# Performance work log

Hardware: AMD Instinct MI355X
Metric: run time of the kernel (lower is better)

The kernel has to match this reference:

```python
import jax, jax.numpy as jnp
import numpy as np

B, L, H, N, NL = 32, 512, 768, 64, 4
GAIN = 1.0


def layer_norm(x, w, b, eps=1e-5):
    mu = jnp.mean(x, axis=-1, keepdims=True)
    var = jnp.mean((x - mu) ** 2, axis=-1, keepdims=True)
    return (x - mu) * jax.lax.rsqrt(var + eps) * w + b


def setup_inputs() -> dict:
    key = jax.random.key(0)
    ks = jax.random.split(key, 10)
    x = jax.random.normal(ks[0], (B, L, H), dtype=jnp.float32)
    mask = jnp.ones((B, L), dtype=jnp.int32)
    # S4D parameters per layer (stacked over NL)
    log_dt = jnp.log(10.0 ** jax.random.uniform(ks[1], (NL, H), minval=-3.0, maxval=-1.0))
    A_re = jnp.zeros((NL, H, N), dtype=jnp.float32)  # real part = -exp(0) = -1
    A_im = jnp.broadcast_to(np.pi * jnp.arange(N, dtype=jnp.float32), (NL, H, N)).copy()
    C_re = jax.random.normal(ks[2], (NL, 2, H, N), dtype=jnp.float32) * 0.5 ** 0.5
    C_im = jax.random.normal(ks[3], (NL, 2, H, N), dtype=jnp.float32) * 0.5 ** 0.5
    D = jax.random.normal(ks[4], (NL, H), dtype=jnp.float32)
    Wout = jax.random.normal(ks[5], (NL, H, H), dtype=jnp.float32) / np.sqrt(H)
    bout = jnp.zeros((NL, H), dtype=jnp.float32)
    ln1_w = jnp.ones((NL, H), dtype=jnp.float32)
    ln1_b = jnp.zeros((NL, H), dtype=jnp.float32)
    ln2_w = jnp.ones((NL, H), dtype=jnp.float32)
    ln2_b = jnp.zeros((NL, H), dtype=jnp.float32)
    return dict(x=x, mask=mask, ln1_w=ln1_w, ln1_b=ln1_b, log_dt=log_dt,
                A_re=A_re, A_im=A_im, C_re=C_re, C_im=C_im, D=D,
                Wout=Wout, bout=bout, ln2_w=ln2_w, ln2_b=ln2_b)


def bis4(u, mask_f, log_dt, A_re, A_im, C_re, C_im, D, Wout, bout):
    # u: [B, L, H] (post ln_1); mask_f: [B, L] float
    u = (u * mask_f[:, :, None]).transpose(0, 2, 1)  # [B, H, L]
    dt = jnp.exp(log_dt)  # [H]
    A = (-jnp.exp(A_re) + 1j * A_im).astype(jnp.complex64)  # [H, N]
    dtA = dt[:, None] * A  # [H, N]
    C = (C_re + 1j * C_im).astype(jnp.complex64)  # [2, H, N]
    # ZOH-style: K[d,h,l] = 2 Re sum_n C (e^{dtA}-1)/A * e^{dtA l}
    Cw = C * ((jnp.exp(dtA) - 1.0) / A)  # [2, H, N]
    V = jnp.exp(dtA[:, :, None] * jnp.arange(L, dtype=jnp.float32))  # [H, N, L]
    K = 2.0 * jnp.real(jnp.einsum('dhn,hnl->dhl', Cw, V))  # [2, H, L]
    # bidirectional kernel over circular length 2L
    k_full = (jnp.pad(K[0], ((0, 0), (0, L))) +
              jnp.pad(K[1, :, ::-1], ((0, 0), (L, 0))))  # [H, 2L]
    kf = jnp.fft.rfft(k_full, n=2 * L)           # [H, L+1]
    uf = jnp.fft.rfft(u, n=2 * L)                # [B, H, L+1]
    y = jnp.fft.irfft(uf * kf, n=2 * L)[..., :L]  # [B, H, L]
    y = y + D[:, None] * u
    y = jax.nn.gelu(y)
    y = y.transpose(0, 2, 1)  # [B, L, H]
    return jnp.einsum('blh,oh->blo', y, Wout) + bout


def reference(x, mask, ln1_w, ln1_b, log_dt, A_re, A_im, C_re, C_im, D, Wout, bout, ln2_w, ln2_b):
    mask_f = mask.astype(x.dtype)
    for i in range(NL):
        y = layer_norm(x, ln1_w[i], ln1_b[i])
        y = bis4(y, mask_f, log_dt[i], A_re[i], A_im[i], C_re[i], C_im[i], D[i], Wout[i], bout[i])
        y = layer_norm(y, ln2_w[i], ln2_b[i])
        x = x + y * GAIN
    return x
```

## Files before the change

### kernel.cpp

```cpp
#include <hip/hip_runtime.h>
#include <math.h>

#define BB 32
#define LL 512
#define HH 768
#define NN 64
#define NLAYERS 4

typedef unsigned short ushort;
typedef __attribute__((ext_vector_type(8))) short bf16x8;
typedef __attribute__((ext_vector_type(4))) float f32x4;
typedef __attribute__((ext_vector_type(4))) ushort u16x4;

static __device__ __forceinline__ ushort f2bf(float f) {
  union { float f; unsigned u; } v; v.f = f;
  unsigned r = (v.u + 0x7FFF + ((v.u >> 16) & 1)) >> 16;
  return (ushort)r;
}
static __device__ __forceinline__ float bf2f(ushort u) {
  union { unsigned u; float f; } v; v.u = ((unsigned)u) << 16; return v.f;
}
static __device__ __forceinline__ void gload16(const void* g, void* l) {
  __builtin_amdgcn_global_load_lds(
      (const __attribute__((address_space(1))) unsigned int*)g,
      (__attribute__((address_space(3))) unsigned int*)l, 16, 0, 0);
}
static __device__ __forceinline__ float hw_sin(float f) {
  float r; asm("v_sin_f32 %0, %1" : "=v"(r) : "v"(f)); return r;
}
static __device__ __forceinline__ float hw_cos(float f) {
  float r; asm("v_cos_f32 %0, %1" : "=v"(r) : "v"(f)); return r;
}

__global__ __launch_bounds__(256) void compute_k_kernel(
    const float* __restrict__ log_dt, const float* __restrict__ A_re,
    const float* __restrict__ A_im, const float* __restrict__ C_re,
    const float* __restrict__ C_im, ushort* __restrict__ rev) {
  __shared__ float4 cons[2][64][5];
  __shared__ float red[2][64][17];
  int wid = threadIdx.x >> 6, lane = threadIdx.x & 63;
  int p = wid >> 1, nh = wid & 1;
  int blk = blockIdx.x * 2 + p;
  int il = blk / HH, h = blk - il * HH;
  if (lane < 32) {
    int n = nh * 32 + lane;
    float dt = expf(log_dt[blk]);
    float a_re = -expf(A_re[(size_t)blk * NN + n]);
    float a_im = A_im[(size_t)blk * NN + n];
    float er = dt * a_re, ei = dt * a_im;
    float ea = __builtin_amdgcn_exp2f(er * 1.4426950408889634f);
    float fr = ei * 0.15915494309189535f;
    fr = fr - floorf(fr);
    float sv = hw_sin(fr), cv = hw_cos(fr);
    float qr = ea * cv, qi = ea * sv;
    float e1r = qr - 1.f, e1i = qi;
    float den = a_re * a_re + a_im * a_im;
    float wr = (e1r * a_re + e1i * a_im) / den;
    float wi = (e1i * a_re - e1r * a_im) / den;
    size_t c0 = ((size_t)(il * 2 + 0) * HH + h) * NN + n;
    size_t c1 = ((size_t)(il * 2 + 1) * HH + h) * NN + n;
    float c0r = C_re[c0], c0i = C_im[c0];
    float c1r = C_re[c1], c1i = C_im[c1];
    float c0wr = 2.f * (c0r * wr - c0i * wi), c0wi = 2.f * (c0r * wi + c0i * wr);
    float c1wr = 2.f * (c1r * wr - c1i * wi), c1wi = 2.f * (c1r * wi + c1i * wr);
    float pr = qr, pi = qi;
    float P[6][2];
#pragma unroll
    for (int j = 0; j < 8; ++j) {
      float nr = pr * pr - pi * pi, ni = 2.f * pr * pi;
      pr = nr; pi = ni;
      if (j >= 2) { P[j - 2][0] = pr; P[j - 2][1] = pi; }
    }
    cons[p][n][0] = make_float4(qr, qi, c0wr, c0wi);
    cons[p][n][1] = make_float4(c1wr, c1wi, P[0][0], P[0][1]);
    cons[p][n][2] = make_float4(P[1][0], P[1][1], P[2][0], P[2][1]);
    cons[p][n][3] = make_float4(P[3][0], P[3][1], P[4][0], P[4][1]);
    cons[p][n][4] = make_float4(P[5][0], P[5][1], 0.f, 0.f);
  }
  __syncthreads();
  int t = lane;
  float k0[8], k1[8];
#pragma unroll
  for (int s = 0; s < 8; ++s) { k0[s] = 0.f; k1[s] = 0.f; }
  for (int nn = 0; nn < 32; ++nn) {
    int n = nh * 32 + nn;
    float4 A0 = cons[p][n][0];
    float4 A1 = cons[p][n][1];
    float4 A2 = cons[p][n][2];
    float4 A3 = cons[p][n][3];
    float4 A4 = cons[p][n][4];
    float vr = 1.f, vi = 0.f;
#define MULIF(BIT, PR, PI) { bool c = (t & (BIT)) != 0;                       \
    float nr = vr * (PR) - vi * (PI), ni = vr * (PI) + vi * (PR);             \
    vr = c ? nr : vr; vi = c ? ni : vi; }
    MULIF(1,  A1.z, A1.w)
    MULIF(2,  A2.x, A2.y)
    MULIF(4,  A2.z, A2.w)
    MULIF(8,  A3.x, A3.y)
    MULIF(16, A3.z, A3.w)
    MULIF(32, A4.x, A4.y)
#undef MULIF
#pragma unroll
    for (int s = 0; s < 8; ++s) {
      k0[s] = fmaf(A0.z, vr, fmaf(-A0.w, vi, k0[s]));
      k1[s] = fmaf(A1.x, vr, fmaf(-A1.y, vi, k1[s]));
      float nr = vr * A0.x - vi * A0.y;
      float ni = vr * A0.y + vi * A0.x;
      vr = nr; vi = ni;
    }
  }
  if (nh == 1) {
#pragma unroll
    for (int s = 0; s < 8; ++s) {
      red[p][lane][s] = k0[s];
      red[p][lane][8 + s] = k1[s];
    }
  }
  __syncthreads();
  if (nh == 0) {
#pragma unroll
    for (int s = 0; s < 8; ++s) {
      k0[s] += red[p][lane][s];
      k1[s] += red[p][lane][8 + s];
    }
    ushort* row = rev + ((size_t)blk << 10);
    bf16x8 o0, o1;
#pragma unroll
    for (int i = 0; i < 8; ++i) {
      o0[i] = (short)f2bf(k0[7 - i]);
      o1[i] = (short)f2bf(k1[i]);
    }
    *(bf16x8*)(row + 504 - 8 * t) = o0;
    *(bf16x8*)(row + 512 + 8 * t) = o1;
  }
}

__global__ __launch_bounds__(256) void wcast_kernel(
    const float* __restrict__ W, ushort* __restrict__ Wbf) {
  size_t i = ((size_t)blockIdx.x * 256 + threadIdx.x) * 8;
  float4 a = *(const float4*)&W[i];
  float4 c = *(const float4*)&W[i + 4];
  ushort o[8] = {f2bf(a.x), f2bf(a.y), f2bf(a.z), f2bf(a.w),
                 f2bf(c.x), f2bf(c.y), f2bf(c.z), f2bf(c.w)};
  *(bf16x8*)&Wbf[i] = *(bf16x8*)o;
}

__global__ __launch_bounds__(256) void ln_t_kernel(
    const float* __restrict__ X, const float* __restrict__ w,
    const float* __restrict__ b, const int* __restrict__ mask,
    ushort* __restrict__ U) {
  __shared__ ushort tile[32][772];
  int bb = blockIdx.y;
  int l0 = blockIdx.x << 5;
  int wv = threadIdx.x >> 6, lane = threadIdx.x & 63;
  const float4* w4 = (const float4*)w;
  const float4* b4 = (const float4*)b;
  float4 WW[3], BV[3];
#pragma unroll
  for (int m = 0; m < 3; ++m) { WW[m] = w4[lane + 64 * m]; BV[m] = b4[lane + 64 * m]; }
#pragma unroll
  for (int i = 0; i < 8; ++i) {
    int r = (wv << 3) + i;
    size_t rowi = (size_t)bb * LL + l0 + r;
    const float4* xr = (const float4*)(X + rowi * HH);
    float4 v[3];
    float s = 0.f, s2 = 0.f;
#pragma unroll
    for (int m = 0; m < 3; ++m) {
      v[m] = xr[lane + 64 * m];
      s  += v[m].x + v[m].y + v[m].z + v[m].w;
      s2 += v[m].x * v[m].x + v[m].y * v[m].y + v[m].z * v[m].z + v[m].w * v[m].w;
    }
#pragma unroll
    for (int off = 32; off >= 1; off >>= 1) {
      s  += __shfl_xor(s, off);
      s2 += __shfl_xor(s2, off);
    }
    float mu  = s * (1.f / HH);
    float var = s2 * (1.f / HH) - mu * mu;
    float rs  = rsqrtf(var + 1e-5f);
    float mf  = (float)mask[rowi];
#pragma unroll
    for (int m = 0; m < 3; ++m) {
      u16x4 o;
      o.x = f2bf(((v[m].x - mu) * rs * WW[m].x + BV[m].x) * mf);
      o.y = f2bf(((v[m].y - mu) * rs * WW[m].y + BV[m].y) * mf);
      o.z = f2bf(((v[m].z - mu) * rs * WW[m].z + BV[m].z) * mf);
      o.w = f2bf(((v[m].w - mu) * rs * WW[m].w + BV[m].w) * mf);
      *(u16x4*)&tile[r][(lane + 64 * m) << 2] = o;
    }
  }
  __syncthreads();
#pragma unroll
  for (int it = 0; it < 3; ++it) {
    int h = it * 256 + threadIdx.x;
    ushort* dst = U + (((size_t)bb * HH + h) << 9) + l0;
#pragma unroll
    for (int c = 0; c < 4; ++c) {
      bf16x8 o;
#pragma unroll
      for (int j = 0; j < 8; ++j) o[j] = (short)tile[c * 8 + j][h];
      *(bf16x8*)(dst + (c << 3)) = o;
    }
  }
}

__global__ __launch_bounds__(256) void res_lnt_kernel(
    const ushort* __restrict__ Gbf, const float* __restrict__ w2,
    const float* __restrict__ b2, const float* __restrict__ base,
    float* __restrict__ out, const int* __restrict__ mask,
    const float* __restrict__ w1, const float* __restrict__ b1,
    ushort* __restrict__ U) {
  __shared__ ushort tile[32][772];
  int bb = blockIdx.y;
  int l0 = blockIdx.x << 5;
  int wv = threadIdx.x >> 6, lane = threadIdx.x & 63;
  const float4* w14 = (const float4*)w1;
  const float4* b14 = (const float4*)b1;
  const float4* w24 = (const float4*)w2;
  const float4* b24 = (const float4*)b2;
  float4 W1[3], B1[3], W2[3], B2[3];
#pragma unroll
  for (int m = 0; m < 3; ++m) {
    W1[m] = w14[lane + 64 * m]; B1[m] = b14[lane + 64 * m];
    W2[m] = w24[lane + 64 * m]; B2[m] = b24[lane + 64 * m];
  }
#pragma unroll
  for (int i = 0; i < 8; ++i) {
    int r = (wv << 3) + i;
    size_t rowi = (size_t)bb * LL + l0 + r;
    const u16x4* gr = (const u16x4*)(Gbf + rowi * HH);
    float gv[12];
    float s = 0.f, s2 = 0.f;
#pragma unroll
    for (int m = 0; m < 3; ++m) {
      u16x4 q = gr[lane + 64 * m];
#pragma unroll
      for (int j = 0; j < 4; ++j) {
        float f = bf2f(q[j]);
        gv[m * 4 + j] = f;
        s += f; s2 += f * f;
      }
    }
#pragma unroll
    for (int off = 32; off >= 1; off >>= 1) {
      s  += __shfl_xor(s, off);
      s2 += __shfl_xor(s2, off);
    }
    float mu2  = s * (1.f / HH);
    float var2 = s2 * (1.f / HH) - mu2 * mu2;
    float rs2  = rsqrtf(var2 + 1e-5f);
    const float4* br = (const float4*)(base + rowi * HH);
    float4* orow = (float4*)(out + rowi * HH);
    float ov[12];
    float t1 = 0.f, t2 = 0.f;
#pragma unroll
    for (int m = 0; m < 3; ++m) {
      float4 bv = br[lane + 64 * m];
      float4 o;
      o.x = bv.x + (gv[m * 4 + 0] - mu2) * rs2 * W2[m].x + B2[m].x;
      o.y = bv.y + (gv[m * 4 + 1] - mu2) * rs2 * W2[m].y + B2[m].y;
      o.z = bv.z + (gv[m * 4 + 2] - mu2) * rs2 * W2[m].z + B2[m].z;
      o.w = bv.w + (gv[m * 4 + 3] - mu2) * rs2 * W2[m].w + B2[m].w;
      orow[lane + 64 * m] = o;
      ov[m * 4 + 0] = o.x; ov[m * 4 + 1] = o.y;
      ov[m * 4 + 2] = o.z; ov[m * 4 + 3] = o.w;
      t1 += o.x + o.y + o.z + o.w;
      t2 += o.x * o.x + o.y * o.y + o.z * o.z + o.w * o.w;
    }
#pragma unroll
    for (int off = 32; off >= 1; off >>= 1) {
      t1 += __shfl_xor(t1, off);
      t2 += __shfl_xor(t2, off);
    }
    float mu1  = t1 * (1.f / HH);
    float var1 = t2 * (1.f / HH) - mu1 * mu1;
    float rs1  = rsqrtf(var1 + 1e-5f);
    float mf   = (float)mask[rowi];
#pragma unroll
    for (int m = 0; m < 3; ++m) {
      u16x4 o;
      o.x = f2bf(((ov[m * 4 + 0] - mu1) * rs1 * W1[m].x + B1[m].x) * mf);
      o.y = f2bf(((ov[m * 4 + 1] - mu1) * rs1 * W1[m].y + B1[m].y) * mf);
      o.z = f2bf(((ov[m * 4 + 2] - mu1) * rs1 * W1[m].z + B1[m].z) * mf);
      o.w = f2bf(((ov[m * 4 + 3] - mu1) * rs1 * W1[m].w + B1[m].w) * mf);
      *(u16x4*)&tile[r][(lane + 64 * m) << 2] = o;
    }
  }
  __syncthreads();
#pragma unroll
  for (int it = 0; it < 3; ++it) {
    int h = it * 256 + threadIdx.x;
    ushort* dst = U + (((size_t)bb * HH + h) << 9) + l0;
#pragma unroll
    for (int c = 0; c < 4; ++c) {
      bf16x8 o;
#pragma unroll
      for (int j = 0; j < 8; ++j) o[j] = (short)tile[c * 8 + j][h];
      *(bf16x8*)(dst + (c << 3)) = o;
    }
  }
}

__global__ __launch_bounds__(256) void ln_res_kernel(
    const ushort* __restrict__ Gbf, const float* __restrict__ w,
    const float* __restrict__ b, const float* __restrict__ base,
    float* __restrict__ out) {
  int wv = threadIdx.x >> 6, lane = threadIdx.x & 63;
  size_t r = (size_t)blockIdx.x * 4 + wv;
  const u16x4* gr = (const u16x4*)(Gbf + r * HH);
  float gv[12];
  float s = 0.f, s2 = 0.f;
#pragma unroll
  for (int m = 0; m < 3; ++m) {
    u16x4 q = gr[lane + 64 * m];
#pragma unroll
    for (int j = 0; j < 4; ++j) {
      float f = bf2f(q[j]);
      gv[m * 4 + j] = f;
      s += f; s2 += f * f;
    }
  }
#pragma unroll
  for (int off = 32; off >= 1; off >>= 1) {
    s  += __shfl_xor(s, off);
    s2 += __shfl_xor(s2, off);
  }
  float mu  = s * (1.f / HH);
  float var = s2 * (1.f / HH) - mu * mu;
  float rs  = rsqrtf(var + 1e-5f);
  const float4* w4 = (const float4*)w;
  const float4* b4 = (const float4*)b;
  const float4* br = (const float4*)(base + r * HH);
  float4* xr = (float4*)(out + r * HH);
#pragma unroll
  for (int m = 0; m < 3; ++m) {
    float4 ww = w4[lane + 64 * m], bb = b4[lane + 64 * m];
    float4 xv = br[lane + 64 * m];
    xv.x += (gv[m * 4 + 0] - mu) * rs * ww.x + bb.x;
    xv.y += (gv[m * 4 + 1] - mu) * rs * ww.y + bb.y;
    xv.z += (gv[m * 4 + 2] - mu) * rs * ww.z + bb.z;
    xv.w += (gv[m * 4 + 3] - mu) * rs * ww.w + bb.w;
    xr[lane + 64 * m] = xv;
  }
}

__global__ __launch_bounds__(256) void conv_mfma_kernel(
    const ushort* __restrict__ Ubf, const ushort* __restrict__ rev,
    const float* __restrict__ Dv, ushort* __restrict__ Cbf) {
  __shared__ ushort Ulds[32 * 512];
  __shared__ ushort Ktab[8 * 1048];
  int tid = threadIdx.x;
  int w = tid >> 6, lane = tid & 63;
  int h = blockIdx.x;

#pragma unroll
  for (int it = 0; it < 8; ++it) {
    int G = it * 256 + tid;
    int b = G >> 6, cg = G & 63;
    gload16(Ubf + (((size_t)b * HH + h) << 9) + ((cg ^ (b & 7)) << 3),
            (char*)Ulds + (size_t)(it * 256 + (tid & 0xFFC0)) * 16);
  }
  const ushort* revh = rev + ((size_t)h << 10);
#pragma unroll
  for (int it = 0; it < 5; ++it) {
    int G = it * 256 + tid;
    if (G < 1048) {
      int r = G / 131, pg = G - r * 131;
      int se = (pg << 3) - 17 - r;
      se = se < 0 ? 0 : (se > 1016 ? 1016 : se);
      gload16(revh + se, (char*)Ktab + (size_t)(it * 256 + (tid & 0xFFC0)) * 16);
    }
  }
  asm volatile("s_waitcnt vmcnt(0)" ::: "memory");
  __syncthreads();

  int cc = lane & 15, g = lane >> 4;
  int wt = w << 7;
  const char* kbase = (const char*)Ktab + (cc & 7) * 2096 - ((cc >> 3) << 4)
                      + (g << 4) + 2 * (528 - wt);
  const char* ubase = (const char*)Ulds;
  int usw = (cc & 7) << 4;

  f32x4 acc[8][2];
#pragma unroll
  for (int m = 0; m < 8; ++m)
#pragma unroll
    for (int n = 0; n < 2; ++n) acc[m][n] = (f32x4){0.f, 0.f, 0.f, 0.f};

  bf16x8 A[8];
#define LDA(slot, m, ks) A[slot] = *(const bf16x8*)(kbase - (m) * 32 + (ks) * 64)
  LDA(0, 0, 0); LDA(1, 1, 0); LDA(2, 2, 0); LDA(3, 3, 0);
  LDA(4, 4, 0); LDA(5, 5, 0); LDA(6, 6, 0); LDA(7, 7, 0);
#pragma unroll
  for (int ks = 0; ks < 16; ++ks) {
    if (ks > 0) {
      LDA((0 - 2 * ks) & 7, 0, ks);
      LDA((1 - 2 * ks) & 7, 1, ks);
    }
    int ub = ((ks << 6) + (g << 4)) ^ usw;
    bf16x8 B0 = *(const bf16x8*)(ubase + cc * 1024 + ub);
    bf16x8 B1 = *(const bf16x8*)(ubase + (16 + cc) * 1024 + ub);
#pragma unroll
    for (int m = 0; m < 8; ++m) {
      acc[m][0] = __builtin_amdgcn_mfma_f32_16x16x32_bf16(
          A[(m - 2 * ks) & 7], B0, acc[m][0], 0, 0, 0);
      acc[m][1] = __builtin_amdgcn_mfma_f32_16x16x32_bf16(
          A[(m - 2 * ks) & 7], B1, acc[m][1], 0, 0, 0);
    }
  }
#undef LDA

  float dh = Dv[h];
  const float c1 = 2.3021181306612f, c3 = 0.1029392186f;
#pragma unroll
  for (int n = 0; n < 2; ++n) {
    int b = (n << 4) + cc;
    const char* up = (const char*)Ulds + b * 1024;
#pragma unroll
    for (int m = 0; m < 8; ++m) {
      int t0 = wt + (m << 4) + (g << 2);
      u16x4 uq = *(const u16x4*)(up + ((t0 << 1) ^ usw));
      u16x4 o;
#pragma unroll
      for (int r = 0; r < 4; ++r) {
        float y = acc[m][n][r] + dh * bf2f(uq[r]);
        float e = __builtin_amdgcn_exp2f(-(c1 * y + c3 * y * y * y));
        float gg = y * __builtin_amdgcn_rcpf(1.f + e);
        o[r] = f2bf(gg);
      }
      *(u16x4*)(Cbf + (((size_t)b * HH + h) << 9) + t0) = o;
    }
  }
}

__global__ __launch_bounds__(256) void t2bf_bf_kernel(
    const ushort* __restrict__ C, ushort* __restrict__ Y) {
  __shared__ ushort tile[32][34];
  int b = blockIdx.z;
  int h0 = blockIdx.x << 5, l0 = blockIdx.y << 5;
  int tx = threadIdx.x, ty = threadIdx.y;
#pragma unroll
  for (int k = 0; k < 4; ++k)
    tile[ty + 8 * k][tx] = C[(((size_t)b * HH + h0 + ty + 8 * k) << 9) + l0 + tx];
  __syncthreads();
#pragma unroll
  for (int k = 0; k < 4; ++k)
    Y[((size_t)b * LL + l0 + ty + 8 * k) * HH + h0 + tx] = tile[tx][ty + 8 * k];
}

__global__ __launch_bounds__(256) void gemm_kernel(
    const ushort* __restrict__ Ybf, const ushort* __restrict__ Wbf,
    const float* __restrict__ bias, ushort* __restrict__ Gb) {
  __shared__ ushort As[128 * 64];
  __shared__ ushort Bs[128 * 64];
  int tid = threadIdx.x;
  int wv = tid >> 6, lane = tid & 63;
  int wm = wv >> 1, wn = wv & 1;
  int b  = blockIdx.y >> 2;
  int l0 = (blockIdx.y & 3) << 7;
  int o0 = blockIdx.x << 7;

  int swz8 = (((lane & 7) ^ (lane >> 3)) << 3);
  int rsub = (lane >> 3);
  size_t arow0 = (size_t)(b * LL + l0 + wv * 32 + rsub) * HH;
  size_t brow0 = (size_t)(o0 + wv * 32 + rsub) * HH;
  char* Adst = (char*)As + wv * 4096;
  char* Bdst = (char*)Bs + wv * 4096;

  f32x4 acc[4][4];
#pragma unroll
  for (int i = 0; i < 4; ++i)
#pragma unroll
    for (int j = 0; j < 4; ++j) acc[i][j] = (f32x4){0.f, 0.f, 0.f, 0.f};

  for (int kt = 0; kt < HH / 64; ++kt) {
    int h0 = kt * 64;
#pragma unroll
    for (int i = 0; i < 4; ++i) {
      gload16(Ybf + arow0 + (size_t)i * 8 * HH + h0 + swz8, Adst + i * 1024);
      gload16(Wbf + brow0 + (size_t)i * 8 * HH + h0 + swz8, Bdst + i * 1024);
    }
    __syncthreads();

    bf16x8 af[4][2], bfr[4][2];
#pragma unroll
    for (int mi = 0; mi < 4; ++mi) {
      int m = wm * 64 + mi * 16 + (lane & 15);
#pragma unroll
      for (int kk = 0; kk < 2; ++kk) {
        int off = m * 128 + ((((lane >> 4) << 4) + (kk << 6)) ^ ((lane & 7) << 4));
        af[mi][kk] = *(const bf16x8*)((const char*)As + off);
      }
    }
#pragma unroll
    for (int ni = 0; ni < 4; ++ni) {
      int n = wn * 64 + ni * 16 + (lane & 15);
#pragma unroll
      for (int kk = 0; kk < 2; ++kk) {
        int off = n * 128 + ((((lane >> 4) << 4) + (kk << 6)) ^ ((lane & 7) << 4));
        bfr[ni][kk] = *(const bf16x8*)((const char*)Bs + off);
      }
    }
#pragma unroll
    for (int kk = 0; kk < 2; ++kk)
#pragma unroll
      for (int mi = 0; mi < 4; ++mi)
#pragma unroll
        for (int ni = 0; ni < 4; ++ni)
          acc[mi][ni] = __builtin_amdgcn_mfma_f32_16x16x32_bf16(
              af[mi][kk], bfr[ni][kk], acc[mi][ni], 0, 0, 0);
    __syncthreads();
  }

#pragma unroll
  for (int ni = 0; ni < 4; ++ni) {
    int n_g = o0 + wn * 64 + ni * 16 + (lane & 15);
    float bv = bias[n_g];
#pragma unroll
    for (int mi = 0; mi < 4; ++mi) {
      int m_g = l0 + wm * 64 + mi * 16 + ((lane >> 4) << 2);
      ushort* gp = Gb + ((size_t)b * LL + m_g) * HH + n_g;
#pragma unroll
      for (int j = 0; j < 4; ++j)
        gp[(size_t)j * HH] = f2bf(acc[mi][ni][j] + bv);
    }
  }
}

extern "C" void kernel_launch(void* const* d_in, const int* in_sizes, int n_in,
                              void* d_out, int out_size, void* d_ws, size_t ws_size,
                              hipStream_t stream) {
  const float* x      = (const float*)d_in[0];
  const int*   mask   = (const int*)d_in[1];
  const float* ln1_w  = (const float*)d_in[2];
  const float* ln1_b  = (const float*)d_in[3];
  const float* log_dt = (const float*)d_in[4];
  const float* A_re   = (const float*)d_in[5];
  const float* A_im   = (const float*)d_in[6];
  const float* C_re   = (const float*)d_in[7];
  const float* C_im   = (const float*)d_in[8];
  const float* Dv     = (const float*)d_in[9];
  const float* Wout   = (const float*)d_in[10];
  const float* bout   = (const float*)d_in[11];
  const float* ln2_w  = (const float*)d_in[12];
  const float* ln2_b  = (const float*)d_in[13];
  float* out = (float*)d_out;

  ushort* rev  = (ushort*)d_ws;
  ushort* Ubf  = rev + (size_t)NLAYERS * HH * 1024;
  ushort* Cbf  = Ubf + (size_t)BB * HH * LL;
  ushort* Wbf  = Cbf + (size_t)BB * HH * LL;
  ushort* Gbf  = Wbf + (size_t)NLAYERS * HH * HH;
  ushort* Ybf  = Ubf;

  compute_k_kernel<<<NLAYERS * HH / 2, 256, 0, stream>>>(
      log_dt, A_re, A_im, C_re, C_im, rev);
  wcast_kernel<<<(NLAYERS * HH * HH) / (256 * 8), 256, 0, stream>>>(Wout, Wbf);

  ln_t_kernel<<<dim3(LL / 32, BB), 256, 0, stream>>>(
      x, ln1_w, ln1_b, mask, Ubf);

  for (int il = 0; il < NLAYERS; ++il) {
    const float* base = (il == 0) ? x : out;
    conv_mfma_kernel<<<HH, 256, 0, stream>>>(
        Ubf, rev + (size_t)il * HH * 1024, Dv + il * HH, Cbf);
    t2bf_bf_kernel<<<dim3(HH / 32, LL / 32, BB), dim3(32, 8), 0, stream>>>(Cbf, Ybf);
    gemm_kernel<<<dim3(HH / 128, BB * LL / 128), 256, 0, stream>>>(
        Ybf, Wbf + (size_t)il * HH * HH, bout + il * HH, Gbf);
    if (il < NLAYERS - 1) {
      res_lnt_kernel<<<dim3(LL / 32, BB), 256, 0, stream>>>(
          Gbf, ln2_w + il * HH, ln2_b + il * HH, base, out,
          mask, ln1_w + (il + 1) * HH, ln1_b + (il + 1) * HH, Ubf);
    } else {
      ln_res_kernel<<<BB * LL / 4, 256, 0, stream>>>(
          Gbf, ln2_w + il * HH, ln2_b + il * HH, base, out);
    }
  }
}
```

Baseline: 526.6 us.

## Keep residual stream in bf16 and restructure S4D kernel generation across waves

The inter-layer residual buffer is stored as bf16 instead of fp32, halving the read and write traffic of the residual/layernorm kernels. The final layer reads the bf16 residual and writes the fp32 output. The kernel-generation step now assigns one head per block, with four waves precomputing power tables in LDS instead of per-lane conditional complex multiplies. This risks accuracy loss from accumulating the residual in bf16 across layers.

```diff
diff --git a/kernel.cpp b/kernel.cpp
--- a/kernel.cpp
+++ b/kernel.cpp
@@ -36,14 +36,16 @@
     const float* __restrict__ log_dt, const float* __restrict__ A_re,
     const float* __restrict__ A_im, const float* __restrict__ C_re,
     const float* __restrict__ C_im, ushort* __restrict__ rev) {
-  __shared__ float4 cons[2][64][5];
-  __shared__ float red[2][64][17];
-  int wid = threadIdx.x >> 6, lane = threadIdx.x & 63;
-  int p = wid >> 1, nh = wid & 1;
-  int blk = blockIdx.x * 2 + p;
+  __shared__ float vr_[64 * 64];
+  __shared__ float vi_[64 * 64];
+  __shared__ float ctab[64][8];
+  __shared__ float red[3][64][17];
+  int tid = threadIdx.x;
+  int wid = tid >> 6, lane = tid & 63;
+  int blk = blockIdx.x;
   int il = blk / HH, h = blk - il * HH;
-  if (lane < 32) {
-    int n = nh * 32 + lane;
+  {
+    int n = lane;
     float dt = expf(log_dt[blk]);
     float a_re = -expf(A_re[(size_t)blk * NN + n]);
     float a_im = A_im[(size_t)blk * NN + n];
@@ -53,76 +55,80 @@
     fr = fr - floorf(fr);
     float sv = hw_sin(fr), cv = hw_cos(fr);
     float qr = ea * cv, qi = ea * sv;
-    float e1r = qr - 1.f, e1i = qi;
-    float den = a_re * a_re + a_im * a_im;
-    float wr = (e1r * a_re + e1i * a_im) / den;
-    float wi = (e1i * a_re - e1r * a_im) / den;
-    size_t c0 = ((size_t)(il * 2 + 0) * HH + h) * NN + n;
-    size_t c1 = ((size_t)(il * 2 + 1) * HH + h) * NN + n;
-    float c0r = C_re[c0], c0i = C_im[c0];
-    float c1r = C_re[c1], c1i = C_im[c1];
-    float c0wr = 2.f * (c0r * wr - c0i * wi), c0wi = 2.f * (c0r * wi + c0i * wr);
-    float c1wr = 2.f * (c1r * wr - c1i * wi), c1wi = 2.f * (c1r * wi + c1i * wr);
+    if (wid == 0) {
+      float e1r = qr - 1.f, e1i = qi;
+      float den = a_re * a_re + a_im * a_im;
+      float wr = (e1r * a_re + e1i * a_im) / den;
+      float wi = (e1i * a_re - e1r * a_im) / den;
+      size_t c0 = ((size_t)(il * 2 + 0) * HH + h) * NN + n;
+      size_t c1 = ((size_t)(il * 2 + 1) * HH + h) * NN + n;
+      float c0r = C_re[c0], c0i = C_im[c0];
+      float c1r = C_re[c1], c1i = C_im[c1];
+      ctab[n][0] = qr; ctab[n][1] = qi;
+      ctab[n][2] = 2.f * (c0r * wr - c0i * wi);
+      ctab[n][3] = 2.f * (c0r * wi + c0i * wr);
+      ctab[n][4] = 2.f * (c1r * wr - c1i * wi);
+      ctab[n][5] = 2.f * (c1r * wi + c1i * wr);
+    }
     float pr = qr, pi = qi;
-    float P[6][2];
+    float q8r = 0.f, q8i = 0.f, q128r = 0.f, q128i = 0.f, q256r = 0.f, q256i = 0.f;
 #pragma unroll
     for (int j = 0; j < 8; ++j) {
       float nr = pr * pr - pi * pi, ni = 2.f * pr * pi;
       pr = nr; pi = ni;
-      if (j >= 2) { P[j - 2][0] = pr; P[j - 2][1] = pi; }
-    }
-    cons[p][n][0] = make_float4(qr, qi, c0wr, c0wi);
-    cons[p][n][1] = make_float4(c1wr, c1wi, P[0][0], P[0][1]);
-    cons[p][n][2] = make_float4(P[1][0], P[1][1], P[2][0], P[2][1]);
-    cons[p][n][3] = make_float4(P[3][0], P[3][1], P[4][0], P[4][1]);
-    cons[p][n][4] = make_float4(P[5][0], P[5][1], 0.f, 0.f);
+      if (j == 2) { q8r = pr; q8i = pi; }
+      if (j == 6) { q128r = pr; q128i = pi; }
+      if (j == 7) { q256r = pr; q256i = pi; }
+    }
+    float sr, si;
+    if (wid == 0)      { sr = 1.f;   si = 0.f; }
+    else if (wid == 1) { sr = q128r; si = q128i; }
+    else if (wid == 2) { sr = q256r; si = q256i; }
+    else { sr = q128r * q256r - q128i * q256i; si = q128r * q256i + q128i * q256r; }
+#pragma unroll
+    for (int j = 0; j < 16; ++j) {
+      int t = wid * 16 + j;
+      vr_[t * 64 + (n ^ t)] = sr;
+      vi_[t * 64 + (n ^ t)] = si;
+      float nr = sr * q8r - si * q8i, ni = sr * q8i + si * q8r;
+      sr = nr; si = ni;
+    }
   }
   __syncthreads();
+  float k0[8], k1[8];
+#pragma unroll
+  for (int s = 0; s < 8; ++s) { k0[s] = 0.f; k1[s] = 0.f; }
   int t = lane;
-  float k0[8], k1[8];
-#pragma unroll
-  for (int s = 0; s < 8; ++s) { k0[s] = 0.f; k1[s] = 0.f; }
-  for (int nn = 0; nn < 32; ++nn) {
-    int n = nh * 32 + nn;
-    float4 A0 = cons[p][n][0];
-    float4 A1 = cons[p][n][1];
-    float4 A2 = cons[p][n][2];
-    float4 A3 = cons[p][n][3];
-    float4 A4 = cons[p][n][4];
-    float vr = 1.f, vi = 0.f;
-#define MULIF(BIT, PR, PI) { bool c = (t & (BIT)) != 0;                       \
-    float nr = vr * (PR) - vi * (PI), ni = vr * (PI) + vi * (PR);             \
-    vr = c ? nr : vr; vi = c ? ni : vi; }
-    MULIF(1,  A1.z, A1.w)
-    MULIF(2,  A2.x, A2.y)
-    MULIF(4,  A2.z, A2.w)
-    MULIF(8,  A3.x, A3.y)
-    MULIF(16, A3.z, A3.w)
-    MULIF(32, A4.x, A4.y)
-#undef MULIF
+  for (int nn = 0; nn < 16; ++nn) {
+    int n = wid * 16 + nn;
+    float4 cA = *(const float4*)&ctab[n][0];
+    float c1wr = ctab[n][4], c1wi = ctab[n][5];
+    float vr = vr_[t * 64 + (n ^ t)];
+    float vi = vi_[t * 64 + (n ^ t)];
 #pragma unroll
     for (int s = 0; s < 8; ++s) {
-      k0[s] = fmaf(A0.z, vr, fmaf(-A0.w, vi, k0[s]));
-      k1[s] = fmaf(A1.x, vr, fmaf(-A1.y, vi, k1[s]));
-      float nr = vr * A0.x - vi * A0.y;
-      float ni = vr * A0.y + vi * A0.x;
+      k0[s] = fmaf(cA.z, vr, fmaf(-cA.w, vi, k0[s]));
+      k1[s] = fmaf(c1wr, vr, fmaf(-c1wi, vi, k1[s]));
+      float nr = vr * cA.x - vi * cA.y, ni = vr * cA.y + vi * cA.x;
       vr = nr; vi = ni;
     }
   }
-  if (nh == 1) {
+  if (wid > 0) {
 #pragma unroll
     for (int s = 0; s < 8; ++s) {
-      red[p][lane][s] = k0[s];
-      red[p][lane][8 + s] = k1[s];
+      red[wid - 1][lane][s] = k0[s];
+      red[wid - 1][lane][8 + s] = k1[s];
     }
   }
   __syncthreads();
-  if (nh == 0) {
-#pragma unroll
-    for (int s = 0; s < 8; ++s) {
-      k0[s] += red[p][lane][s];
-      k1[s] += red[p][lane][8 + s];
-    }
+  if (wid == 0) {
+#pragma unroll
+    for (int w = 0; w < 3; ++w)
+#pragma unroll
+      for (int s = 0; s < 8; ++s) {
+        k0[s] += red[w][lane][s];
+        k1[s] += red[w][lane][8 + s];
+      }
     ushort* row = rev + ((size_t)blk << 10);
     bf16x8 o0, o1;
 #pragma unroll
@@ -205,10 +211,11 @@
   }
 }
 
+template <bool BASE_F32>
 __global__ __launch_bounds__(256) void res_lnt_kernel(
     const ushort* __restrict__ Gbf, const float* __restrict__ w2,
-    const float* __restrict__ b2, const float* __restrict__ base,
-    float* __restrict__ out, const int* __restrict__ mask,
+    const float* __restrict__ b2, const void* __restrict__ base_,
+    ushort* __restrict__ outbf, const int* __restrict__ mask,
     const float* __restrict__ w1, const float* __restrict__ b1,
     ushort* __restrict__ U) {
   __shared__ ushort tile[32][772];
@@ -250,23 +257,29 @@
     float mu2  = s * (1.f / HH);
     float var2 = s2 * (1.f / HH) - mu2 * mu2;
     float rs2  = rsqrtf(var2 + 1e-5f);
-    const float4* br = (const float4*)(base + rowi * HH);
-    float4* orow = (float4*)(out + rowi * HH);
     float ov[12];
     float t1 = 0.f, t2 = 0.f;
 #pragma unroll
     for (int m = 0; m < 3; ++m) {
-      float4 bv = br[lane + 64 * m];
-      float4 o;
-      o.x = bv.x + (gv[m * 4 + 0] - mu2) * rs2 * W2[m].x + B2[m].x;
-      o.y = bv.y + (gv[m * 4 + 1] - mu2) * rs2 * W2[m].y + B2[m].y;
-      o.z = bv.z + (gv[m * 4 + 2] - mu2) * rs2 * W2[m].z + B2[m].z;
-      o.w = bv.w + (gv[m * 4 + 3] - mu2) * rs2 * W2[m].w + B2[m].w;
-      orow[lane + 64 * m] = o;
-      ov[m * 4 + 0] = o.x; ov[m * 4 + 1] = o.y;
-      ov[m * 4 + 2] = o.z; ov[m * 4 + 3] = o.w;
-      t1 += o.x + o.y + o.z + o.w;
-      t2 += o.x * o.x + o.y * o.y + o.z * o.z + o.w * o.w;
+      float bvv[4];
+      if (BASE_F32) {
+        float4 bv = ((const float4*)((const float*)base_ + rowi * HH))[lane + 64 * m];
+        bvv[0] = bv.x; bvv[1] = bv.y; bvv[2] = bv.z; bvv[3] = bv.w;
+      } else {
+        u16x4 bq = ((const u16x4*)((const ushort*)base_ + rowi * HH))[lane + 64 * m];
+#pragma unroll
+        for (int j = 0; j < 4; ++j) bvv[j] = bf2f(bq[j]);
+      }
+      u16x4 ob;
+#pragma unroll
+      for (int j = 0; j < 4; ++j) {
+        float o = bvv[j] + (gv[m * 4 + j] - mu2) * rs2 * ((const float*)&W2[m])[j]
+                  + ((const float*)&B2[m])[j];
+        ov[m * 4 + j] = o;
+        ob[j] = f2bf(o);
+        t1 += o; t2 += o * o;
+      }
+      ((u16x4*)(outbf + rowi * HH))[lane + 64 * m] = ob;
     }
 #pragma unroll
     for (int off = 32; off >= 1; off >>= 1) {
@@ -304,7 +317,7 @@
 
 __global__ __launch_bounds__(256) void ln_res_kernel(
     const ushort* __restrict__ Gbf, const float* __restrict__ w,
-    const float* __restrict__ b, const float* __restrict__ base,
+    const float* __restrict__ b, const ushort* __restrict__ basebf,
     float* __restrict__ out) {
   int wv = threadIdx.x >> 6, lane = threadIdx.x & 63;
   size_t r = (size_t)blockIdx.x * 4 + wv;
@@ -331,16 +344,17 @@
   float rs  = rsqrtf(var + 1e-5f);
   const float4* w4 = (const float4*)w;
   const float4* b4 = (const float4*)b;
-  const float4* br = (const float4*)(base + r * HH);
+  const u16x4* br = (const u16x4*)(basebf + r * HH);
   float4* xr = (float4*)(out + r * HH);
 #pragma unroll
   for (int m = 0; m < 3; ++m) {
     float4 ww = w4[lane + 64 * m], bb = b4[lane + 64 * m];
-    float4 xv = br[lane + 64 * m];
-    xv.x += (gv[m * 4 + 0] - mu) * rs * ww.x + bb.x;
-    xv.y += (gv[m * 4 + 1] - mu) * rs * ww.y + bb.y;
-    xv.z += (gv[m * 4 + 2] - mu) * rs * ww.z + bb.z;
-    xv.w += (gv[m * 4 + 3] - mu) * rs * ww.w + bb.w;
+    u16x4 bq = br[lane + 64 * m];
+    float4 xv;
+    xv.x = bf2f(bq[0]) + (gv[m * 4 + 0] - mu) * rs * ww.x + bb.x;
+    xv.y = bf2f(bq[1]) + (gv[m * 4 + 1] - mu) * rs * ww.y + bb.y;
+    xv.z = bf2f(bq[2]) + (gv[m * 4 + 2] - mu) * rs * ww.z + bb.z;
+    xv.w = bf2f(bq[3]) + (gv[m * 4 + 3] - mu) * rs * ww.w + bb.w;
     xr[lane + 64 * m] = xv;
   }
 }
@@ -552,9 +566,10 @@
   ushort* Cbf  = Ubf + (size_t)BB * HH * LL;
   ushort* Wbf  = Cbf + (size_t)BB * HH * LL;
   ushort* Gbf  = Wbf + (size_t)NLAYERS * HH * HH;
+  ushort* Obf  = Gbf + (size_t)BB * LL * HH;
   ushort* Ybf  = Ubf;
 
-  compute_k_kernel<<<NLAYERS * HH / 2, 256, 0, stream>>>(
+  compute_k_kernel<<<NLAYERS * HH, 256, 0, stream>>>(
       log_dt, A_re, A_im, C_re, C_im, rev);
   wcast_kernel<<<(NLAYERS * HH * HH) / (256 * 8), 256, 0, stream>>>(Wout, Wbf);
 
@@ -562,19 +577,21 @@
       x, ln1_w, ln1_b, mask, Ubf);
 
   for (int il = 0; il < NLAYERS; ++il) {
-    const float* base = (il == 0) ? x : out;
     conv_mfma_kernel<<<HH, 256, 0, stream>>>(
         Ubf, rev + (size_t)il * HH * 1024, Dv + il * HH, Cbf);
     t2bf_bf_kernel<<<dim3(HH / 32, LL / 32, BB), dim3(32, 8), 0, stream>>>(Cbf, Ybf);
     gemm_kernel<<<dim3(HH / 128, BB * LL / 128), 256, 0, stream>>>(
         Ybf, Wbf + (size_t)il * HH * HH, bout + il * HH, Gbf);
-    if (il < NLAYERS - 1) {
-      res_lnt_kernel<<<dim3(LL / 32, BB), 256, 0, stream>>>(
-          Gbf, ln2_w + il * HH, ln2_b + il * HH, base, out,
-          mask, ln1_w + (il + 1) * HH, ln1_b + (il + 1) * HH, Ubf);
+    if (il == 0) {
+      res_lnt_kernel<true><<<dim3(LL / 32, BB), 256, 0, stream>>>(
+          Gbf, ln2_w, ln2_b, x, Obf, mask, ln1_w + HH, ln1_b + HH, Ubf);
+    } else if (il < NLAYERS - 1) {
+      res_lnt_kernel<false><<<dim3(LL / 32, BB), 256, 0, stream>>>(
+          Gbf, ln2_w + il * HH, ln2_b + il * HH, Obf, Obf, mask,
+          ln1_w + (il + 1) * HH, ln1_b + (il + 1) * HH, Ubf);
     } else {
       ln_res_kernel<<<BB * LL / 4, 256, 0, stream>>>(
-          Gbf, ln2_w + il * HH, ln2_b + il * HH, base, out);
-    }
-  }
-}
+          Gbf, ln2_w + il * HH, ln2_b + il * HH, Obf, out);
+    }
+  }
+}
```

Result: slower. 560.3 us (+6.4%).
